# Performance work log

Hardware: AMD Instinct MI355X
Metric: run time of the kernel (lower is better)

## Reference

```python
import jax, jax.numpy as jnp
import numpy as np

B, NQ, NN, EMB, H, D = 64, 256, 512, 128, 8, 16
SQRT_EMB = float(np.sqrt(EMB))
LOGIT_CLIP = 10.0


def setup_inputs() -> dict:
    key = jax.random.key(0)
    ks = jax.random.split(key, 9)
    encoded_last_node = jax.random.normal(ks[0], (B, NQ, EMB), jnp.float32)
    attr = jax.random.uniform(ks[1], (B, NQ, 1), jnp.float32)  # e.g. remaining load in [0,1]
    encoded_nodes = jax.random.normal(ks[2], (B, NN, EMB), jnp.float32)
    ninf_mask = jnp.where(jax.random.uniform(ks[3], (B, NQ, NN)) < 0.15,
                          -jnp.inf, 0.0).astype(jnp.float32)
    def lin(k, fan_in, fan_out):
        lim = 1.0 / np.sqrt(fan_in)
        return jax.random.uniform(k, (fan_in, fan_out), jnp.float32, -lim, lim)
    Wq_last = lin(ks[4], EMB + 1, H * D)
    Wk = lin(ks[5], EMB, H * D)
    Wv = lin(ks[6], EMB, H * D)
    Wcomb = lin(ks[7], H * D, EMB)
    bcomb = jax.random.uniform(ks[8], (EMB,), jnp.float32, -1.0 / np.sqrt(H * D), 1.0 / np.sqrt(H * D))
    return dict(encoded_last_node=encoded_last_node, attr=attr,
                encoded_nodes=encoded_nodes, ninf_mask=ninf_mask,
                Wq_last=Wq_last, Wk=Wk, Wv=Wv, Wcomb=Wcomb, bcomb=bcomb)


def _heads(x):  # [B, T, H*D] -> [B, H, T, D]
    return x.reshape(x.shape[0], x.shape[1], H, D).transpose(0, 2, 1, 3)


def reference(encoded_last_node, attr, encoded_nodes, ninf_mask,
              Wq_last, Wk, Wv, Wcomb, bcomb):
    # fix fully-masked rows: un-mask index 0 (matches torch mask_inf patch)
    all_inf = jnp.isinf(ninf_mask).all(axis=2)  # [B, NQ]
    ninf_mask = ninf_mask.at[:, :, 0].set(jnp.where(all_inf, 0.0, ninf_mask[:, :, 0]))

    # set_kv
    k = _heads(encoded_nodes @ Wk)  # [B,H,NN,D]
    v = _heads(encoded_nodes @ Wv)  # [B,H,NN,D]

    # q from last node + attr
    q = _heads(jnp.concatenate([encoded_last_node, attr], axis=2) @ Wq_last)  # [B,H,NQ,D]

    # masked multi-head attention
    score = jnp.einsum('bhnd,bhmd->bhnm', q, k) / jnp.sqrt(jnp.float32(D))
    score = score + ninf_mask[:, None, :, :]          # rank3 mask broadcast over heads
    weights = jax.nn.softmax(score, axis=-1)          # [B,H,NQ,NN]
    out = jnp.einsum('bhnm,bhmd->bhnd', weights, v)
    out_concat = out.transpose(0, 2, 1, 3).reshape(B, NQ, H * D)
    mh_atten_out = out_concat @ Wcomb + bcomb         # [B,NQ,EMB]

    # single-head compatibility score + tanh clip + mask + softmax
    score2 = jnp.einsum('bne,bme->bnm', mh_atten_out, encoded_nodes) / SQRT_EMB
    logits = LOGIT_CLIP * jnp.tanh(score2) + ninf_mask
    probs = jax.nn.softmax(logits, axis=2)            # [B,NQ,NN]
    return probs
```

## Files before the change

kernel.cpp:

```cpp
#include <hip/hip_runtime.h>
#include <math.h>

#define NB    64
#define NQn   256
#define NNn   512
#define HDn   128
#define LOG2E 1.44269504088896340736f
#define INV_SQRT_EMB 0.08838834764831845f

__device__ __forceinline__ float4 ldg4(const float* p) {
    return *reinterpret_cast<const float4*>(p);
}

__global__ __launch_bounds__(256, 4)
void mask_transpose(const float* __restrict__ mask, unsigned char* __restrict__ maskT8)
{
    const int tid = threadIdx.x;
    const int w   = tid >> 6;
    const int n   = blockIdx.z * 64 + (tid & 63);
    const int b   = blockIdx.x;
    const int q0  = blockIdx.y * 64 + w * 16;
    unsigned int u[4] = {0u, 0u, 0u, 0u};
    #pragma unroll
    for (int j = 0; j < 16; ++j) {
        float v = mask[((size_t)(b * NQn + q0 + j)) * NNn + n];
        unsigned int bit = (v != 0.0f) ? 1u : 0u;
        u[j >> 2] |= bit << (8 * (j & 3));
    }
    *reinterpret_cast<uint4*>(maskT8 + ((size_t)(b * NNn + n)) * NQn + q0) =
        make_uint4(u[0], u[1], u[2], u[3]);
}

__global__ __launch_bounds__(256, 2)
void proj_kernel(const float* __restrict__ X,
                 const float* __restrict__ W0, const float* __restrict__ W1,
                 const float* __restrict__ wrow, const float* __restrict__ attr,
                 const float* __restrict__ bias,
                 float* __restrict__ Y0, float* __restrict__ Y1)
{
    __shared__ float Xs[64 * 128];
    __shared__ float Wt[64 * 128];
    const int tid = threadIdx.x;
    const int rg = tid >> 4;
    const int cg = tid & 15;
    const int rowblk = blockIdx.x * 64;
    const int colbase = blockIdx.y * 64;

    #pragma unroll
    for (int i = 0; i < 8; ++i) {
        int idx = tid + 256 * i;
        int r = idx >> 5;
        int c4 = idx & 31;
        float4 v = ldg4(X + (rowblk + r) * 128 + c4 * 4);
        *reinterpret_cast<float4*>(&Xs[r * 128 + ((c4 ^ (r & 7)) << 2)]) = v;
    }

    for (int pass = 0; pass < 2; ++pass) {
        if (pass && (W1 == nullptr)) break;
        const float* W = pass ? W1 : W0;
        float* Y = pass ? Y1 : Y0;
        __syncthreads();
        #pragma unroll
        for (int i = 0; i < 32; ++i) {
            int idx = tid + 256 * i;
            int k = idx >> 6;
            int c = idx & 63;
            float w = W[k * 128 + colbase + c];
            Wt[c * 128 + ((((k >> 2) ^ (c & 7)) << 2) | (k & 3))] = w;
        }
        __syncthreads();

        float acc[4][4];
        #pragma unroll
        for (int r = 0; r < 4; ++r)
            #pragma unroll
            for (int c = 0; c < 4; ++c) acc[r][c] = 0.f;

        const int rsw = rg & 7;
        const int csw = cg & 7;
        #pragma unroll 8
        for (int k4 = 0; k4 < 32; ++k4) {
            float4 a[4], bv[4];
            #pragma unroll
            for (int r = 0; r < 4; ++r)
                a[r] = *reinterpret_cast<const float4*>(&Xs[(rg + 16 * r) * 128 + ((k4 ^ rsw) << 2)]);
            #pragma unroll
            for (int c = 0; c < 4; ++c)
                bv[c] = *reinterpret_cast<const float4*>(&Wt[(cg + 16 * c) * 128 + ((k4 ^ csw) << 2)]);
            #pragma unroll
            for (int r = 0; r < 4; ++r)
                #pragma unroll
                for (int c = 0; c < 4; ++c)
                    acc[r][c] += a[r].x * bv[c].x + a[r].y * bv[c].y
                               + a[r].z * bv[c].z + a[r].w * bv[c].w;
        }

        if (attr != nullptr) {
            #pragma unroll
            for (int r = 0; r < 4; ++r) {
                float av = attr[rowblk + rg + 16 * r];
                #pragma unroll
                for (int c = 0; c < 4; ++c)
                    acc[r][c] += av * wrow[colbase + cg + 16 * c];
            }
        }
        #pragma unroll
        for (int r = 0; r < 4; ++r) {
            int row = rowblk + rg + 16 * r;
            #pragma unroll
            for (int c = 0; c < 4; ++c) {
                int col = colbase + cg + 16 * c;
                float o = acc[r][c];
                if (bias != nullptr) o += bias[col];
                Y[row * 128 + col] = o;
            }
        }
    }
}

__global__ __launch_bounds__(512, 2)
void attn_kernel(const float* __restrict__ Q, const float* __restrict__ K,
                 const float* __restrict__ V, const unsigned int* __restrict__ maskTu,
                 float* __restrict__ P0, float* __restrict__ P1,
                 float* __restrict__ P2, float* __restrict__ P3,
                 float* __restrict__ L0, float* __restrict__ L1,
                 float* __restrict__ L2, float* __restrict__ L3)
{
    __shared__ float Ks[32 * 128];
    __shared__ float Vs[32 * 128];
    const int tid  = threadIdx.x;
    const int lane = tid & 63;
    const int h    = tid >> 6;
    const int b    = blockIdx.x;
    const int ns   = blockIdx.y;
    const int nbase = ns * 128;

    float qv[4][16];
    {
        const float sc = 0.25f * LOG2E;
        #pragma unroll
        for (int qq = 0; qq < 4; ++qq) {
            const float* qp = Q + ((size_t)(b * NQn + 4 * lane + qq)) * 128 + h * 16;
            #pragma unroll
            for (int j = 0; j < 4; ++j) {
                float4 tv = ldg4(qp + 4 * j);
                qv[qq][4 * j + 0] = tv.x * sc;
                qv[qq][4 * j + 1] = tv.y * sc;
                qv[qq][4 * j + 2] = tv.z * sc;
                qv[qq][4 * j + 3] = tv.w * sc;
            }
        }
    }

    float out[4][16];
    #pragma unroll
    for (int qq = 0; qq < 4; ++qq)
        #pragma unroll
        for (int d = 0; d < 16; ++d) out[qq][d] = 0.f;
    float ls[4] = {0.f, 0.f, 0.f, 0.f};

    const unsigned int* mbase = maskTu + (((size_t)(b * NNn + nbase) * NQn) >> 2) + lane;

    for (int t = 0; t < 4; ++t) {
        __syncthreads();
        {
            const float* kg = K + ((size_t)(b * NNn + nbase + t * 32)) * 128;
            const float* vg = V + ((size_t)(b * NNn + nbase + t * 32)) * 128;
            float4 k0 = ldg4(kg + tid * 4);
            float4 k1 = ldg4(kg + (tid + 512) * 4);
            float4 v0 = ldg4(vg + tid * 4);
            float4 v1 = ldg4(vg + (tid + 512) * 4);
            *reinterpret_cast<float4*>(&Ks[tid * 4]) = k0;
            *reinterpret_cast<float4*>(&Ks[(tid + 512) * 4]) = k1;
            *reinterpret_cast<float4*>(&Vs[tid * 4]) = v0;
            *reinterpret_cast<float4*>(&Vs[(tid + 512) * 4]) = v1;
        }
        __syncthreads();

        const float* kbase = &Ks[h * 16];
        const float* vbase = &Vs[h * 16];
        for (int n = 0; n < 32; ++n) {
            const float* kr = kbase + n * 128;
            const float* vr = vbase + n * 128;
            float kf[16], vf[16];
            *reinterpret_cast<float4*>(&kf[0])  = *reinterpret_cast<const float4*>(kr);
            *reinterpret_cast<float4*>(&kf[4])  = *reinterpret_cast<const float4*>(kr + 4);
            *reinterpret_cast<float4*>(&kf[8])  = *reinterpret_cast<const float4*>(kr + 8);
            *reinterpret_cast<float4*>(&kf[12]) = *reinterpret_cast<const float4*>(kr + 12);
            *reinterpret_cast<float4*>(&vf[0])  = *reinterpret_cast<const float4*>(vr);
            *reinterpret_cast<float4*>(&vf[4])  = *reinterpret_cast<const float4*>(vr + 4);
            *reinterpret_cast<float4*>(&vf[8])  = *reinterpret_cast<const float4*>(vr + 8);
            *reinterpret_cast<float4*>(&vf[12]) = *reinterpret_cast<const float4*>(vr + 12);
            unsigned int m4 = mbase[(t * 32 + n) * (NQn / 4)];

            float p[4];
            #pragma unroll
            for (int qq = 0; qq < 4; ++qq) {
                float aP = qv[qq][0]*kf[0] + qv[qq][1]*kf[1] + qv[qq][2]*kf[2] + qv[qq][3]*kf[3];
                float aQ = qv[qq][4]*kf[4] + qv[qq][5]*kf[5] + qv[qq][6]*kf[6] + qv[qq][7]*kf[7];
                float aR = qv[qq][8]*kf[8] + qv[qq][9]*kf[9] + qv[qq][10]*kf[10] + qv[qq][11]*kf[11];
                float aS = qv[qq][12]*kf[12] + qv[qq][13]*kf[13] + qv[qq][14]*kf[14] + qv[qq][15]*kf[15];
                p[qq] = exp2f((aP + aQ) + (aR + aS));
            }
            p[0] = (m4 & 0x000000ffu) ? 0.f : p[0];
            p[1] = (m4 & 0x0000ff00u) ? 0.f : p[1];
            p[2] = (m4 & 0x00ff0000u) ? 0.f : p[2];
            p[3] = (m4 & 0xff000000u) ? 0.f : p[3];
            ls[0] += p[0]; ls[1] += p[1]; ls[2] += p[2]; ls[3] += p[3];
            #pragma unroll
            for (int d = 0; d < 16; ++d) {
                out[0][d] += p[0] * vf[d];
                out[1][d] += p[1] * vf[d];
                out[2][d] += p[2] * vf[d];
                out[3][d] += p[3] * vf[d];
            }
        }
    }

    float* P = (ns == 0) ? P0 : (ns == 1) ? P1 : (ns == 2) ? P2 : P3;
    float* L = (ns == 0) ? L0 : (ns == 1) ? L1 : (ns == 2) ? L2 : L3;
    #pragma unroll
    for (int qq = 0; qq < 4; ++qq) {
        float* op = P + ((size_t)(b * NQn + 4 * lane + qq)) * 128 + h * 16;
        *reinterpret_cast<float4*>(op)      = make_float4(out[qq][0],  out[qq][1],  out[qq][2],  out[qq][3]);
        *reinterpret_cast<float4*>(op + 4)  = make_float4(out[qq][4],  out[qq][5],  out[qq][6],  out[qq][7]);
        *reinterpret_cast<float4*>(op + 8)  = make_float4(out[qq][8],  out[qq][9],  out[qq][10], out[qq][11]);
        *reinterpret_cast<float4*>(op + 12) = make_float4(out[qq][12], out[qq][13], out[qq][14], out[qq][15]);
        L[(b * NQn + 4 * lane + qq) * 8 + h] = ls[qq];
    }
}

__global__ __launch_bounds__(256, 4)
void attn_merge(const float* __restrict__ P0, const float* __restrict__ P1,
                const float* __restrict__ P2, const float* __restrict__ P3,
                const float* __restrict__ L0, const float* __restrict__ L1,
                const float* __restrict__ L2, const float* __restrict__ L3,
                const float* __restrict__ V, float* __restrict__ ATT)
{
    const int idx = blockIdx.x * 256 + threadIdx.x;
    const int row = idx >> 5;
    const int f4i = idx & 31;
    const int hh  = f4i >> 2;
    const int b   = row >> 8;
    const float l = (L0[row * 8 + hh] + L1[row * 8 + hh])
                  + (L2[row * 8 + hh] + L3[row * 8 + hh]);
    float4 a = ldg4(P0 + (size_t)row * 128 + f4i * 4);
    float4 c = ldg4(P1 + (size_t)row * 128 + f4i * 4);
    float4 d = ldg4(P2 + (size_t)row * 128 + f4i * 4);
    float4 e = ldg4(P3 + (size_t)row * 128 + f4i * 4);
    float4 r;
    if (l == 0.0f) {
        r = ldg4(V + (size_t)b * NNn * 128 + f4i * 4);
    } else {
        float inv = __builtin_amdgcn_rcpf(l);
        r = make_float4((a.x + c.x + d.x + e.x) * inv, (a.y + c.y + d.y + e.y) * inv,
                        (a.z + c.z + d.z + e.z) * inv, (a.w + c.w + d.w + e.w) * inv);
    }
    *reinterpret_cast<float4*>(ATT + (size_t)row * 128 + f4i * 4) = r;
}

__global__ __launch_bounds__(512, 2)
void final_kernel(const float* __restrict__ MH, const float* __restrict__ EN,
                  const float* __restrict__ mask, float* __restrict__ OUT)
{
    __shared__ float ENs[128 * 128];
    const int tid = threadIdx.x;
    const int qg = tid >> 4;
    const int mg = tid & 15;
    const int b  = blockIdx.x >> 2;
    const int q0 = (blockIdx.x & 3) * 64;

    const float* mhbase = MH + (b * NQn + q0) * 128;
    float pr[2][32];
    float psum[2] = {0.f, 0.f};
    const int msw = mg & 7;

    #pragma unroll
    for (int t = 0; t < 4; ++t) {
        const int m0 = t * 128;
        __syncthreads();
        #pragma unroll
        for (int i = 0; i < 8; ++i) {
            int idx = tid + 512 * i;
            int r = idx >> 5;
            int c4 = idx & 31;
            float4 v = ldg4(EN + (b * NNn + m0 + r) * 128 + c4 * 4);
            *reinterpret_cast<float4*>(&ENs[r * 128 + ((c4 ^ (r & 7)) << 2)]) = v;
        }
        __syncthreads();

        float acc[2][8];
        #pragma unroll
        for (int qq = 0; qq < 2; ++qq)
            #pragma unroll
            for (int c = 0; c < 8; ++c) acc[qq][c] = 0.f;

        #pragma unroll 4
        for (int k4 = 0; k4 < 32; ++k4) {
            float4 a0 = ldg4(mhbase + (qg * 2 + 0) * 128 + k4 * 4);
            float4 a1 = ldg4(mhbase + (qg * 2 + 1) * 128 + k4 * 4);
            float4 bv[8];
            #pragma unroll
            for (int c = 0; c < 8; ++c)
                bv[c] = *reinterpret_cast<const float4*>(&ENs[(mg + 16 * c) * 128 + ((k4 ^ msw) << 2)]);
            #pragma unroll
            for (int c = 0; c < 8; ++c) {
                acc[0][c] += a0.x*bv[c].x + a0.y*bv[c].y + a0.z*bv[c].z + a0.w*bv[c].w;
                acc[1][c] += a1.x*bv[c].x + a1.y*bv[c].y + a1.z*bv[c].z + a1.w*bv[c].w;
            }
        }

        #pragma unroll
        for (int qq = 0; qq < 2; ++qq) {
            const int q = q0 + qg * 2 + qq;
            const float* mrow = mask + (b * NQn + q) * NNn + m0;
            #pragma unroll
            for (int c = 0; c < 8; ++c) {
                int m = mg + 16 * c;
                float s2 = acc[qq][c] * INV_SQRT_EMB;
                float e  = exp2f(s2 * (2.0f * LOG2E));
                float rc = __builtin_amdgcn_rcpf(e + 1.0f);
                float mv = mrow[m];
                float pv = exp2f((mv - 20.0f * rc) * LOG2E);
                pr[qq][t * 8 + c] = pv;
                psum[qq] += pv;
            }
        }
    }

    #pragma unroll
    for (int qq = 0; qq < 2; ++qq) {
        float s = psum[qq];
        s += __shfl_xor(s, 1);
        s += __shfl_xor(s, 2);
        s += __shfl_xor(s, 4);
        s += __shfl_xor(s, 8);
        psum[qq] = s;
    }

    #pragma unroll
    for (int qq = 0; qq < 2; ++qq) {
        const int q = q0 + qg * 2 + qq;
        float* orow = OUT + (b * NQn + q) * NNn;
        if (psum[qq] == 0.0f) {
            #pragma unroll
            for (int t = 0; t < 4; ++t)
                #pragma unroll
                for (int c = 0; c < 8; ++c) {
                    int m = t * 128 + mg + 16 * c;
                    orow[m] = (m == 0) ? 1.0f : 0.0f;
                }
        } else {
            float inv = __builtin_amdgcn_rcpf(psum[qq]);
            #pragma unroll
            for (int t = 0; t < 4; ++t)
                #pragma unroll
                for (int c = 0; c < 8; ++c)
                    orow[t * 128 + mg + 16 * c] = pr[qq][t * 8 + c] * inv;
        }
    }
}

extern "C" void kernel_launch(void* const* d_in, const int* in_sizes, int n_in,
                              void* d_out, int out_size, void* d_ws, size_t ws_size,
                              hipStream_t stream) {
    const float* enc_last  = (const float*)d_in[0];
    const float* attr      = (const float*)d_in[1];
    const float* enc_nodes = (const float*)d_in[2];
    const float* mask      = (const float*)d_in[3];
    const float* Wq        = (const float*)d_in[4];
    const float* Wk        = (const float*)d_in[5];
    const float* Wv        = (const float*)d_in[6];
    const float* Wcomb     = (const float*)d_in[7];
    const float* bcomb     = (const float*)d_in[8];
    float* out = (float*)d_out;

    float* Kbuf = (float*)d_ws;
    float* Vbuf = Kbuf + (size_t)NB * NNn * 128;
    float* Qbuf = Vbuf + (size_t)NB * NNn * 128;
    float* ATT  = Qbuf + (size_t)NB * NQn * 128;
    float* P1   = ATT  + (size_t)NB * NQn * 128;
    float* P2   = P1   + (size_t)NB * NQn * 128;
    float* P3   = P2   + (size_t)NB * NQn * 128;
    float* L0   = P3   + (size_t)NB * NQn * 128;
    float* L1   = L0   + (size_t)NB * NQn * 8;
    float* L2   = L1   + (size_t)NB * NQn * 8;
    float* L3   = L2   + (size_t)NB * NQn * 8;
    unsigned char* maskT8 = (unsigned char*)(L3 + (size_t)NB * NQn * 8);
    float* MH   = P1;

    mask_transpose<<<dim3(NB, NQn / 64, NNn / 64), 256, 0, stream>>>(mask, maskT8);
    proj_kernel<<<dim3(NB * NNn / 64, 2), 256, 0, stream>>>(
        enc_nodes, Wk, Wv, nullptr, nullptr, nullptr, Kbuf, Vbuf);
    proj_kernel<<<dim3(NB * NQn / 64, 2), 256, 0, stream>>>(
        enc_last, Wq, nullptr, Wq + 128 * 128, attr, nullptr, Qbuf, nullptr);
    attn_kernel<<<dim3(NB, 4), 512, 0, stream>>>(
        Qbuf, Kbuf, Vbuf, (const unsigned int*)maskT8,
        ATT, P1, P2, P3, L0, L1, L2, L3);
    attn_merge<<<dim3(NB * NQn * 32 / 256), 256, 0, stream>>>(
        ATT, P1, P2, P3, L0, L1, L2, L3, Vbuf, ATT);
    proj_kernel<<<dim3(NB * NQn / 64, 2), 256, 0, stream>>>(
        ATT, Wcomb, nullptr, nullptr, nullptr, bcomb, MH, nullptr);
    final_kernel<<<dim3(NB * NQn / 64), 512, 0, stream>>>(
        MH, enc_nodes, mask, out);
}
```

Measured before the change: 246.7 us.

## Split attention queries across two block tiles and raise occupancy

The attention kernel grid gains a query-tile dimension, so each thread handles 2 queries instead of 4 and twice as many blocks launch (64x2x4). Launch bounds rise to 4 blocks per SM, which cuts per-thread registers so that more waves can hide latency. Mask reads become 16-bit loads, and exp2 now runs only for unmasked entries. In exchange, each K/V tile in shared memory is loaded twice as often, reuse per load drops, and the MH buffer alias moves to Qbuf.

```diff
diff --git a/kernel.cpp b/kernel.cpp
--- a/kernel.cpp
+++ b/kernel.cpp
@@ -118,9 +118,9 @@
     }
 }
 
-__global__ __launch_bounds__(512, 2)
+__global__ __launch_bounds__(512, 4)
 void attn_kernel(const float* __restrict__ Q, const float* __restrict__ K,
-                 const float* __restrict__ V, const unsigned int* __restrict__ maskTu,
+                 const float* __restrict__ V, const unsigned char* __restrict__ maskT8,
                  float* __restrict__ P0, float* __restrict__ P1,
                  float* __restrict__ P2, float* __restrict__ P3,
                  float* __restrict__ L0, float* __restrict__ L1,
@@ -132,34 +132,35 @@
     const int lane = tid & 63;
     const int h    = tid >> 6;
     const int b    = blockIdx.x;
-    const int ns   = blockIdx.y;
+    const int qt   = blockIdx.y;
+    const int ns   = blockIdx.z;
+    const int q0   = qt * 128 + 2 * lane;
     const int nbase = ns * 128;
 
-    float qv[4][16];
+    float qv[2][16];
     {
         const float sc = 0.25f * LOG2E;
         #pragma unroll
-        for (int qq = 0; qq < 4; ++qq) {
-            const float* qp = Q + ((size_t)(b * NQn + 4 * lane + qq)) * 128 + h * 16;
+        for (int qq = 0; qq < 2; ++qq) {
+            const float* qp = Q + ((size_t)(b * NQn + q0 + qq)) * 128 + h * 16;
             #pragma unroll
             for (int j = 0; j < 4; ++j) {
                 float4 tv = ldg4(qp + 4 * j);
-                qv[qq][4 * j + 0] = tv.x * sc;
-                qv[qq][4 * j + 1] = tv.y * sc;
-                qv[qq][4 * j + 2] = tv.z * sc;
-                qv[qq][4 * j + 3] = tv.w * sc;
+                qv[qq][4*j+0] = tv.x * sc; qv[qq][4*j+1] = tv.y * sc;
+                qv[qq][4*j+2] = tv.z * sc; qv[qq][4*j+3] = tv.w * sc;
             }
         }
     }
 
-    float out[4][16];
-    #pragma unroll
-    for (int qq = 0; qq < 4; ++qq)
+    float out[2][16];
+    #pragma unroll
+    for (int qq = 0; qq < 2; ++qq)
         #pragma unroll
         for (int d = 0; d < 16; ++d) out[qq][d] = 0.f;
-    float ls[4] = {0.f, 0.f, 0.f, 0.f};
-
-    const unsigned int* mbase = maskTu + (((size_t)(b * NNn + nbase) * NQn) >> 2) + lane;
+    float ls0 = 0.f, ls1 = 0.f;
+
+    const unsigned short* mb = reinterpret_cast<const unsigned short*>(
+        maskT8 + ((size_t)(b * NNn + nbase)) * NQn + q0);
 
     for (int t = 0; t < 4; ++t) {
         __syncthreads();
@@ -168,10 +169,10 @@
             const float* vg = V + ((size_t)(b * NNn + nbase + t * 32)) * 128;
             float4 k0 = ldg4(kg + tid * 4);
             float4 k1 = ldg4(kg + (tid + 512) * 4);
+            *reinterpret_cast<float4*>(&Ks[tid * 4]) = k0;
+            *reinterpret_cast<float4*>(&Ks[(tid + 512) * 4]) = k1;
             float4 v0 = ldg4(vg + tid * 4);
             float4 v1 = ldg4(vg + (tid + 512) * 4);
-            *reinterpret_cast<float4*>(&Ks[tid * 4]) = k0;
-            *reinterpret_cast<float4*>(&Ks[(tid + 512) * 4]) = k1;
             *reinterpret_cast<float4*>(&Vs[tid * 4]) = v0;
             *reinterpret_cast<float4*>(&Vs[(tid + 512) * 4]) = v1;
         }
@@ -180,53 +181,47 @@
         const float* kbase = &Ks[h * 16];
         const float* vbase = &Vs[h * 16];
         for (int n = 0; n < 32; ++n) {
-            const float* kr = kbase + n * 128;
-            const float* vr = vbase + n * 128;
-            float kf[16], vf[16];
-            *reinterpret_cast<float4*>(&kf[0])  = *reinterpret_cast<const float4*>(kr);
-            *reinterpret_cast<float4*>(&kf[4])  = *reinterpret_cast<const float4*>(kr + 4);
-            *reinterpret_cast<float4*>(&kf[8])  = *reinterpret_cast<const float4*>(kr + 8);
-            *reinterpret_cast<float4*>(&kf[12]) = *reinterpret_cast<const float4*>(kr + 12);
-            *reinterpret_cast<float4*>(&vf[0])  = *reinterpret_cast<const float4*>(vr);
-            *reinterpret_cast<float4*>(&vf[4])  = *reinterpret_cast<const float4*>(vr + 4);
-            *reinterpret_cast<float4*>(&vf[8])  = *reinterpret_cast<const float4*>(vr + 8);
-            *reinterpret_cast<float4*>(&vf[12]) = *reinterpret_cast<const float4*>(vr + 12);
-            unsigned int m4 = mbase[(t * 32 + n) * (NQn / 4)];
-
-            float p[4];
-            #pragma unroll
-            for (int qq = 0; qq < 4; ++qq) {
-                float aP = qv[qq][0]*kf[0] + qv[qq][1]*kf[1] + qv[qq][2]*kf[2] + qv[qq][3]*kf[3];
-                float aQ = qv[qq][4]*kf[4] + qv[qq][5]*kf[5] + qv[qq][6]*kf[6] + qv[qq][7]*kf[7];
-                float aR = qv[qq][8]*kf[8] + qv[qq][9]*kf[9] + qv[qq][10]*kf[10] + qv[qq][11]*kf[11];
-                float aS = qv[qq][12]*kf[12] + qv[qq][13]*kf[13] + qv[qq][14]*kf[14] + qv[qq][15]*kf[15];
-                p[qq] = exp2f((aP + aQ) + (aR + aS));
-            }
-            p[0] = (m4 & 0x000000ffu) ? 0.f : p[0];
-            p[1] = (m4 & 0x0000ff00u) ? 0.f : p[1];
-            p[2] = (m4 & 0x00ff0000u) ? 0.f : p[2];
-            p[3] = (m4 & 0xff000000u) ? 0.f : p[3];
-            ls[0] += p[0]; ls[1] += p[1]; ls[2] += p[2]; ls[3] += p[3];
-            #pragma unroll
-            for (int d = 0; d < 16; ++d) {
-                out[0][d] += p[0] * vf[d];
-                out[1][d] += p[1] * vf[d];
-                out[2][d] += p[2] * vf[d];
-                out[3][d] += p[3] * vf[d];
-            }
+            unsigned int m2 = mb[(size_t)(t * 32 + n) * 128];
+            float4 k0 = *reinterpret_cast<const float4*>(kbase + n * 128);
+            float4 k1 = *reinterpret_cast<const float4*>(kbase + n * 128 + 4);
+            float4 k2 = *reinterpret_cast<const float4*>(kbase + n * 128 + 8);
+            float4 k3 = *reinterpret_cast<const float4*>(kbase + n * 128 + 12);
+            float s0 = (qv[0][0]*k0.x + qv[0][1]*k0.y + qv[0][2]*k0.z + qv[0][3]*k0.w)
+                     + (qv[0][4]*k1.x + qv[0][5]*k1.y + qv[0][6]*k1.z + qv[0][7]*k1.w)
+                     + (qv[0][8]*k2.x + qv[0][9]*k2.y + qv[0][10]*k2.z + qv[0][11]*k2.w)
+                     + (qv[0][12]*k3.x + qv[0][13]*k3.y + qv[0][14]*k3.z + qv[0][15]*k3.w);
+            float s1 = (qv[1][0]*k0.x + qv[1][1]*k0.y + qv[1][2]*k0.z + qv[1][3]*k0.w)
+                     + (qv[1][4]*k1.x + qv[1][5]*k1.y + qv[1][6]*k1.z + qv[1][7]*k1.w)
+                     + (qv[1][8]*k2.x + qv[1][9]*k2.y + qv[1][10]*k2.z + qv[1][11]*k2.w)
+                     + (qv[1][12]*k3.x + qv[1][13]*k3.y + qv[1][14]*k3.z + qv[1][15]*k3.w);
+            float p0 = (m2 & 0x00ffu) ? 0.f : exp2f(s0);
+            float p1 = (m2 & 0xff00u) ? 0.f : exp2f(s1);
+            ls0 += p0; ls1 += p1;
+            float4 v0 = *reinterpret_cast<const float4*>(vbase + n * 128);
+            float4 v1 = *reinterpret_cast<const float4*>(vbase + n * 128 + 4);
+            float4 v2 = *reinterpret_cast<const float4*>(vbase + n * 128 + 8);
+            float4 v3 = *reinterpret_cast<const float4*>(vbase + n * 128 + 12);
+            out[0][0]  += p0*v0.x; out[0][1]  += p0*v0.y; out[0][2]  += p0*v0.z; out[0][3]  += p0*v0.w;
+            out[0][4]  += p0*v1.x; out[0][5]  += p0*v1.y; out[0][6]  += p0*v1.z; out[0][7]  += p0*v1.w;
+            out[0][8]  += p0*v2.x; out[0][9]  += p0*v2.y; out[0][10] += p0*v2.z; out[0][11] += p0*v2.w;
+            out[0][12] += p0*v3.x; out[0][13] += p0*v3.y; out[0][14] += p0*v3.z; out[0][15] += p0*v3.w;
+            out[1][0]  += p1*v0.x; out[1][1]  += p1*v0.y; out[1][2]  += p1*v0.z; out[1][3]  += p1*v0.w;
+            out[1][4]  += p1*v1.x; out[1][5]  += p1*v1.y; out[1][6]  += p1*v1.z; out[1][7]  += p1*v1.w;
+            out[1][8]  += p1*v2.x; out[1][9]  += p1*v2.y; out[1][10] += p1*v2.z; out[1][11] += p1*v2.w;
+            out[1][12] += p1*v3.x; out[1][13] += p1*v3.y; out[1][14] += p1*v3.z; out[1][15] += p1*v3.w;
         }
     }
 
     float* P = (ns == 0) ? P0 : (ns == 1) ? P1 : (ns == 2) ? P2 : P3;
     float* L = (ns == 0) ? L0 : (ns == 1) ? L1 : (ns == 2) ? L2 : L3;
     #pragma unroll
-    for (int qq = 0; qq < 4; ++qq) {
-        float* op = P + ((size_t)(b * NQn + 4 * lane + qq)) * 128 + h * 16;
+    for (int qq = 0; qq < 2; ++qq) {
+        float* op = P + ((size_t)(b * NQn + q0 + qq)) * 128 + h * 16;
         *reinterpret_cast<float4*>(op)      = make_float4(out[qq][0],  out[qq][1],  out[qq][2],  out[qq][3]);
         *reinterpret_cast<float4*>(op + 4)  = make_float4(out[qq][4],  out[qq][5],  out[qq][6],  out[qq][7]);
         *reinterpret_cast<float4*>(op + 8)  = make_float4(out[qq][8],  out[qq][9],  out[qq][10], out[qq][11]);
         *reinterpret_cast<float4*>(op + 12) = make_float4(out[qq][12], out[qq][13], out[qq][14], out[qq][15]);
-        L[(b * NQn + 4 * lane + qq) * 8 + h] = ls[qq];
+        L[(b * NQn + q0 + qq) * 8 + h] = (qq == 0) ? ls0 : ls1;
     }
 }
 
@@ -387,16 +382,15 @@
     float* L2   = L1   + (size_t)NB * NQn * 8;
     float* L3   = L2   + (size_t)NB * NQn * 8;
     unsigned char* maskT8 = (unsigned char*)(L3 + (size_t)NB * NQn * 8);
-    float* MH   = P1;
+    float* MH   = Qbuf;
 
     mask_transpose<<<dim3(NB, NQn / 64, NNn / 64), 256, 0, stream>>>(mask, maskT8);
     proj_kernel<<<dim3(NB * NNn / 64, 2), 256, 0, stream>>>(
         enc_nodes, Wk, Wv, nullptr, nullptr, nullptr, Kbuf, Vbuf);
     proj_kernel<<<dim3(NB * NQn / 64, 2), 256, 0, stream>>>(
         enc_last, Wq, nullptr, Wq + 128 * 128, attr, nullptr, Qbuf, nullptr);
-    attn_kernel<<<dim3(NB, 4), 512, 0, stream>>>(
-        Qbuf, Kbuf, Vbuf, (const unsigned int*)maskT8,
-        ATT, P1, P2, P3, L0, L1, L2, L3);
+    attn_kernel<<<dim3(NB, 2, 4), 512, 0, stream>>>(
+        Qbuf, Kbuf, Vbuf, maskT8, ATT, P1, P2, P3, L0, L1, L2, L3);
     attn_merge<<<dim3(NB * NQn * 32 / 256), 256, 0, stream>>>(
         ATT, P1, P2, P3, L0, L1, L2, L3, Vbuf, ATT);
     proj_kernel<<<dim3(NB * NQn / 64, 2), 256, 0, stream>>>(
```

New measurement: 266.4 us. +8.0%, slower.

## Prefetch next K/V/mask tile into registers and stage mask in LDS

Applied to the files above, without the earlier changes.

The attention kernel now loads the next 32-row K/V tile and the matching transposed mask bytes into registers while the current tile is computed, so the global-memory latency overlaps with compute. The mask is staged in shared memory per tile instead of being read from global memory inside the inner loop, and that inner loop is fully unrolled. exp2f is replaced with the hardware exp2 builtin, and the MH buffer is aliased to Qbuf instead of P1. In exchange it uses more registers and extra LDS, which could reduce occupancy.

```diff
diff --git a/kernel.cpp b/kernel.cpp
--- a/kernel.cpp
+++ b/kernel.cpp
@@ -120,7 +120,7 @@
 
 __global__ __launch_bounds__(512, 2)
 void attn_kernel(const float* __restrict__ Q, const float* __restrict__ K,
-                 const float* __restrict__ V, const unsigned int* __restrict__ maskTu,
+                 const float* __restrict__ V, const unsigned char* __restrict__ maskT8,
                  float* __restrict__ P0, float* __restrict__ P1,
                  float* __restrict__ P2, float* __restrict__ P3,
                  float* __restrict__ L0, float* __restrict__ L1,
@@ -128,6 +128,7 @@
 {
     __shared__ float Ks[32 * 128];
     __shared__ float Vs[32 * 128];
+    __shared__ unsigned int Ms[32 * 64];
     const int tid  = threadIdx.x;
     const int lane = tid & 63;
     const int h    = tid >> 6;
@@ -144,10 +145,8 @@
             #pragma unroll
             for (int j = 0; j < 4; ++j) {
                 float4 tv = ldg4(qp + 4 * j);
-                qv[qq][4 * j + 0] = tv.x * sc;
-                qv[qq][4 * j + 1] = tv.y * sc;
-                qv[qq][4 * j + 2] = tv.z * sc;
-                qv[qq][4 * j + 3] = tv.w * sc;
+                qv[qq][4*j+0] = tv.x * sc; qv[qq][4*j+1] = tv.y * sc;
+                qv[qq][4*j+2] = tv.z * sc; qv[qq][4*j+3] = tv.w * sc;
             }
         }
     }
@@ -159,39 +158,48 @@
         for (int d = 0; d < 16; ++d) out[qq][d] = 0.f;
     float ls[4] = {0.f, 0.f, 0.f, 0.f};
 
-    const unsigned int* mbase = maskTu + (((size_t)(b * NNn + nbase) * NQn) >> 2) + lane;
+    const float* kg = K + ((size_t)(b * NNn + nbase)) * 128;
+    const float* vg = V + ((size_t)(b * NNn + nbase)) * 128;
+    const unsigned char* mg = maskT8
+        + ((size_t)(b * NNn + nbase) + (tid >> 4)) * NQn + (tid & 15) * 16;
+
+    float4 kr0 = ldg4(kg + tid * 4);
+    float4 kr1 = ldg4(kg + (tid + 512) * 4);
+    float4 vr0 = ldg4(vg + tid * 4);
+    float4 vr1 = ldg4(vg + (tid + 512) * 4);
+    uint4  mr  = *reinterpret_cast<const uint4*>(mg);
 
     for (int t = 0; t < 4; ++t) {
         __syncthreads();
-        {
-            const float* kg = K + ((size_t)(b * NNn + nbase + t * 32)) * 128;
-            const float* vg = V + ((size_t)(b * NNn + nbase + t * 32)) * 128;
-            float4 k0 = ldg4(kg + tid * 4);
-            float4 k1 = ldg4(kg + (tid + 512) * 4);
-            float4 v0 = ldg4(vg + tid * 4);
-            float4 v1 = ldg4(vg + (tid + 512) * 4);
-            *reinterpret_cast<float4*>(&Ks[tid * 4]) = k0;
-            *reinterpret_cast<float4*>(&Ks[(tid + 512) * 4]) = k1;
-            *reinterpret_cast<float4*>(&Vs[tid * 4]) = v0;
-            *reinterpret_cast<float4*>(&Vs[(tid + 512) * 4]) = v1;
-        }
-        __syncthreads();
-
-        const float* kbase = &Ks[h * 16];
-        const float* vbase = &Vs[h * 16];
+        *reinterpret_cast<float4*>(&Ks[tid * 4])         = kr0;
+        *reinterpret_cast<float4*>(&Ks[(tid + 512) * 4]) = kr1;
+        *reinterpret_cast<float4*>(&Vs[tid * 4])         = vr0;
+        *reinterpret_cast<float4*>(&Vs[(tid + 512) * 4]) = vr1;
+        *reinterpret_cast<uint4*>(&Ms[(tid >> 4) * 64 + (tid & 15) * 4]) = mr;
+        __syncthreads();
+        if (t < 3) {
+            kr0 = ldg4(kg + (t + 1) * 4096 + tid * 4);
+            kr1 = ldg4(kg + (t + 1) * 4096 + (tid + 512) * 4);
+            vr0 = ldg4(vg + (t + 1) * 4096 + tid * 4);
+            vr1 = ldg4(vg + (t + 1) * 4096 + (tid + 512) * 4);
+            mr  = *reinterpret_cast<const uint4*>(mg + (size_t)(t + 1) * 32 * NQn);
+        }
+
+        const float* kb = &Ks[h * 16];
+        const float* vb = &Vs[h * 16];
+        const unsigned int* mbL = &Ms[lane];
+        #pragma unroll
         for (int n = 0; n < 32; ++n) {
-            const float* kr = kbase + n * 128;
-            const float* vr = vbase + n * 128;
+            unsigned int m4 = mbL[n * 64];
             float kf[16], vf[16];
-            *reinterpret_cast<float4*>(&kf[0])  = *reinterpret_cast<const float4*>(kr);
-            *reinterpret_cast<float4*>(&kf[4])  = *reinterpret_cast<const float4*>(kr + 4);
-            *reinterpret_cast<float4*>(&kf[8])  = *reinterpret_cast<const float4*>(kr + 8);
-            *reinterpret_cast<float4*>(&kf[12]) = *reinterpret_cast<const float4*>(kr + 12);
-            *reinterpret_cast<float4*>(&vf[0])  = *reinterpret_cast<const float4*>(vr);
-            *reinterpret_cast<float4*>(&vf[4])  = *reinterpret_cast<const float4*>(vr + 4);
-            *reinterpret_cast<float4*>(&vf[8])  = *reinterpret_cast<const float4*>(vr + 8);
-            *reinterpret_cast<float4*>(&vf[12]) = *reinterpret_cast<const float4*>(vr + 12);
-            unsigned int m4 = mbase[(t * 32 + n) * (NQn / 4)];
+            *reinterpret_cast<float4*>(&kf[0])  = *reinterpret_cast<const float4*>(kb + n * 128);
+            *reinterpret_cast<float4*>(&kf[4])  = *reinterpret_cast<const float4*>(kb + n * 128 + 4);
+            *reinterpret_cast<float4*>(&kf[8])  = *reinterpret_cast<const float4*>(kb + n * 128 + 8);
+            *reinterpret_cast<float4*>(&kf[12]) = *reinterpret_cast<const float4*>(kb + n * 128 + 12);
+            *reinterpret_cast<float4*>(&vf[0])  = *reinterpret_cast<const float4*>(vb + n * 128);
+            *reinterpret_cast<float4*>(&vf[4])  = *reinterpret_cast<const float4*>(vb + n * 128 + 4);
+            *reinterpret_cast<float4*>(&vf[8])  = *reinterpret_cast<const float4*>(vb + n * 128 + 8);
+            *reinterpret_cast<float4*>(&vf[12]) = *reinterpret_cast<const float4*>(vb + n * 128 + 12);
 
             float p[4];
             #pragma unroll
@@ -200,7 +208,7 @@
                 float aQ = qv[qq][4]*kf[4] + qv[qq][5]*kf[5] + qv[qq][6]*kf[6] + qv[qq][7]*kf[7];
                 float aR = qv[qq][8]*kf[8] + qv[qq][9]*kf[9] + qv[qq][10]*kf[10] + qv[qq][11]*kf[11];
                 float aS = qv[qq][12]*kf[12] + qv[qq][13]*kf[13] + qv[qq][14]*kf[14] + qv[qq][15]*kf[15];
-                p[qq] = exp2f((aP + aQ) + (aR + aS));
+                p[qq] = __builtin_amdgcn_exp2f((aP + aQ) + (aR + aS));
             }
             p[0] = (m4 & 0x000000ffu) ? 0.f : p[0];
             p[1] = (m4 & 0x0000ff00u) ? 0.f : p[1];
@@ -387,7 +395,7 @@
     float* L2   = L1   + (size_t)NB * NQn * 8;
     float* L3   = L2   + (size_t)NB * NQn * 8;
     unsigned char* maskT8 = (unsigned char*)(L3 + (size_t)NB * NQn * 8);
-    float* MH   = P1;
+    float* MH   = Qbuf;
 
     mask_transpose<<<dim3(NB, NQn / 64, NNn / 64), 256, 0, stream>>>(mask, maskT8);
     proj_kernel<<<dim3(NB * NNn / 64, 2), 256, 0, stream>>>(
@@ -395,8 +403,7 @@
     proj_kernel<<<dim3(NB * NQn / 64, 2), 256, 0, stream>>>(
         enc_last, Wq, nullptr, Wq + 128 * 128, attr, nullptr, Qbuf, nullptr);
     attn_kernel<<<dim3(NB, 4), 512, 0, stream>>>(
-        Qbuf, Kbuf, Vbuf, (const unsigned int*)maskT8,
-        ATT, P1, P2, P3, L0, L1, L2, L3);
+        Qbuf, Kbuf, Vbuf, maskT8, ATT, P1, P2, P3, L0, L1, L2, L3);
     attn_merge<<<dim3(NB * NQn * 32 / 256), 256, 0, stream>>>(
         ATT, P1, P2, P3, L0, L1, L2, L3, Vbuf, ATT);
     proj_kernel<<<dim3(NB * NQn / 64, 2), 256, 0, stream>>>(
```

Result: slower. 728.7 us (+195.3%).
